# Kernel tuning notes

Hardware: AMD Instinct MI355X
Metric: run time of the kernel (lower is better)

## Reference

```python
import jax, jax.numpy as jnp
import numpy as np

N = 100000; E = 1600000; C = 32; H = 2
KS = (3, 3, 5, 5)
NEG = 0.01      # LeakyReLU default slope
GAT_NEG = 0.2   # SuperGAT attention leaky_relu slope
EPS = 1e-5      # BatchNorm eps


def setup_inputs() -> dict:
    key = jax.random.key(0)
    ks = jax.random.split(key, 64)
    inp = {}
    inp["patch_embs"] = jax.random.normal(ks[0], (N, C), dtype=jnp.float32)
    ei = np.array(jax.random.randint(ks[1], (2, E), 0, N))
    # avoid self loops so PyG's remove_self_loops/add_self_loops semantics match exactly
    ei[1] = np.where(ei[0] == ei[1], (ei[1] + 1) % N, ei[1])
    inp["edge_index"] = jnp.array(ei, dtype=jnp.int32)
    inp["edge_attr"] = jax.random.normal(ks[2], (E, 1), dtype=jnp.float32)
    s = 1.0 / np.sqrt(C)
    i = 3
    for b in range(4):
        inp[f"W{b}"] = (jax.random.normal(ks[i], (KS[b], C, C)) * s).astype(jnp.float32); i += 1
        inp[f"cb{b}"] = jnp.zeros((C,), jnp.float32)                     # ChebConv bias
        inp[f"G{b}"] = (jax.random.normal(ks[i], (C, H * C)) * s).astype(jnp.float32); i += 1  # SuperGAT lin
        inp[f"al{b}"] = (jax.random.normal(ks[i], (H, C)) * s).astype(jnp.float32); i += 1     # att_l
        inp[f"ar{b}"] = (jax.random.normal(ks[i], (H, C)) * s).astype(jnp.float32); i += 1     # att_r
        inp[f"gb{b}"] = jnp.zeros((C,), jnp.float32)                     # SuperGAT bias
        inp[f"gm{b}"] = jnp.ones((C,), jnp.float32)                      # BN gamma
        inp[f"bt{b}"] = jnp.zeros((C,), jnp.float32)                     # BN beta
    return inp


def _cheb(x, src, dst, w, W, cb):
    # ChebConv with sym Laplacian, lambda_max=2 -> L_hat = -D^-1/2 A D^-1/2
    def spmv(v):
        return jax.ops.segment_sum(w[:, None] * v[src], dst, num_segments=N)
    tx0, out = x, x @ W[0]
    tx1 = spmv(x)
    out = out + tx1 @ W[1]
    for k in range(2, W.shape[0]):
        tx0, tx1 = tx1, 2.0 * spmv(tx1) - tx0
        out = out + tx1 @ W[k]
    return out + cb


def _supergat(x, ssrc, sdst, G, al, ar, gb):
    # SuperGATConv, attention_type='MX', heads=2, concat=False (mean)
    h = (x @ G).reshape(N, H, C)          # [N,H,C]
    hi, hj = h[sdst], h[ssrc]              # gathered per edge (incl. self loops)
    logits = jnp.sum(hi * hj, -1)          # [Etot,H]
    a = jnp.sum(hj * al, -1) + jnp.sum(hi * ar, -1)
    a = jax.nn.leaky_relu(a * jax.nn.sigmoid(logits), GAT_NEG)
    amax = jax.ops.segment_max(a, sdst, num_segments=N)
    ex = jnp.exp(a - amax[sdst])
    den = jax.ops.segment_sum(ex, sdst, num_segments=N)
    alpha = ex / (den[sdst] + 1e-16)
    out = jax.ops.segment_sum(alpha[..., None] * hj, sdst, num_segments=N)
    return out.mean(axis=1) + gb


def _block(x, src, dst, w, ssrc, sdst, W, cb, G, al, ar, gb, gm, bt):
    s_ = _supergat(_cheb(x, src, dst, w, W, cb), ssrc, sdst, G, al, ar, gb)
    y = jax.nn.leaky_relu(s_, NEG) + s_
    mu = y.mean(0)
    var = y.var(0)  # biased var, matches torch BN training normalization
    return gm * (y - mu) / jnp.sqrt(var + EPS) + bt


def _forward(x, edge_index, params):
    src, dst = edge_index[0], edge_index[1]
    deg = jax.ops.segment_sum(jnp.ones((E,), jnp.float32), src, num_segments=N)
    di = deg[src] * deg[dst]
    w = jnp.where(di > 0, -1.0 / jnp.sqrt(jnp.maximum(di, 1e-12)), 0.0)
    loop = jnp.arange(N, dtype=edge_index.dtype)
    ssrc = jnp.concatenate([src, loop])
    sdst = jnp.concatenate([dst, loop])
    acc = 0.0
    for b in range(4):
        W, cb, G, al, ar, gb, gm, bt = params[b]
        acc = acc + _block(x, src, dst, w, ssrc, sdst, W, cb, G, al, ar, gb, gm, bt)
    return jax.nn.leaky_relu(acc, NEG)


def reference(patch_embs, edge_index, edge_attr,
              W0, cb0, G0, al0, ar0, gb0, gm0, bt0,
              W1, cb1, G1, al1, ar1, gb1, gm1, bt1,
              W2, cb2, G2, al2, ar2, gb2, gm2, bt2,
              W3, cb3, G3, al3, ar3, gb3, gm3, bt3):
    params = [(W0, cb0, G0, al0, ar0, gb0, gm0, bt0),
              (W1, cb1, G1, al1, ar1, gb1, gm1, bt1),
              (W2, cb2, G2, al2, ar2, gb2, gm2, bt2),
              (W3, cb3, G3, al3, ar3, gb3, gm3, bt3)]
    return _forward(patch_embs, edge_index, params)
```

## Files before the change

kernel.cpp:

```cpp
#include <hip/hip_runtime.h>
#include <math.h>

#define NN 100000
#define EE 1600000
#define CCH 32
#define NC (NN*CCH)
#define ET (EE+NN)
#define NEGS 0.01f
#define GNEG 0.2f
#define BEPS 1e-5f


__global__ void k_degs(const int* __restrict__ src, const int* __restrict__ dst,
                       float* __restrict__ deg_out, int* __restrict__ indeg){
    int e = blockIdx.x*blockDim.x + threadIdx.x;
    if (e >= EE) return;
    atomicAdd(&deg_out[src[e]], 1.0f);
    atomicAdd(&indeg[dst[e]], 1);
}

#define SCAN_T 1024
__global__ void k_scan(const int* __restrict__ indeg, int* __restrict__ row){
    __shared__ int sdata[SCAN_T];
    int t = threadIdx.x;
    const int per = (NN + SCAN_T - 1)/SCAN_T;
    int lo = t*per, hi = (lo + per < NN) ? lo + per : NN;
    int s = 0;
    for (int d = lo; d < hi; d++) s += indeg[d] + 1;
    sdata[t] = s;
    __syncthreads();
    for (int off = 1; off < SCAN_T; off <<= 1){
        int v = (t >= off) ? sdata[t-off] : 0;
        __syncthreads();
        sdata[t] += v;
        __syncthreads();
    }
    int excl = (t == 0) ? 0 : sdata[t-1];
    for (int d = lo; d < hi; d++){
        row[d] = excl;
        excl += indeg[d] + 1;
    }
    if (t == 0) row[NN] = ET;
}

__global__ void k_self(const int* __restrict__ row, int* __restrict__ csr_src,
                       float* __restrict__ csr_w){
    int d = blockIdx.x*blockDim.x + threadIdx.x;
    if (d >= NN) return;
    int p = row[d];
    csr_src[p] = d;
    csr_w[p] = 0.0f;
}

__global__ void k_scatter(const int* __restrict__ src, const int* __restrict__ dst,
                          const float* __restrict__ deg_out, const int* __restrict__ row,
                          int* __restrict__ cur, int* __restrict__ csr_src,
                          float* __restrict__ csr_w){
    int e = blockIdx.x*blockDim.x + threadIdx.x;
    if (e >= EE) return;
    int s = src[e], d = dst[e];
    int pos = row[d] + 1 + atomicAdd(&cur[d], 1);
    csr_src[pos] = s;
    float di = deg_out[s] * deg_out[d];
    csr_w[pos] = (di > 0.0f) ? (-1.0f / sqrtf(fmaxf(di, 1e-12f))) : 0.0f;
}

__global__ void k_spmv_csr(const int* __restrict__ row, const int* __restrict__ csr_src,
                           const float* __restrict__ csr_w, const float* __restrict__ v,
                           const float* __restrict__ tprev, float* __restrict__ out, int first){
    int gid = blockIdx.x*blockDim.x + threadIdx.x;
    int node = gid >> 6;
    if (node >= NN) return;
    int lane = gid & 63;
    int slot = lane >> 4;
    int l = lane & 15;
    const float2* V2 = (const float2*)v;
    int start = row[node] + 1, end = row[node+1];
    float2 acc = {0.0f, 0.0f};
    int p = start + slot;
    for (; p + 4 < end; p += 8){
        int s0 = csr_src[p], s1 = csr_src[p+4];
        float w0 = csr_w[p], w1 = csr_w[p+4];
        float2 v0 = V2[(size_t)s0*16 + l];
        float2 v1 = V2[(size_t)s1*16 + l];
        acc.x += w0*v0.x + w1*v1.x;
        acc.y += w0*v0.y + w1*v1.y;
    }
    if (p < end){
        float w0 = csr_w[p];
        float2 v0 = V2[(size_t)csr_src[p]*16 + l];
        acc.x += w0*v0.x;
        acc.y += w0*v0.y;
    }
    acc.x += __shfl_xor(acc.x, 32); acc.y += __shfl_xor(acc.y, 32);
    acc.x += __shfl_xor(acc.x, 16); acc.y += __shfl_xor(acc.y, 16);
    if (slot == 0){
        float2 r;
        if (first){
            r = acc;
        } else {
            float2 t = ((const float2*)tprev)[(size_t)node*16 + l];
            r.x = 2.0f*acc.x - t.x;
            r.y = 2.0f*acc.y - t.y;
        }
        ((float2*)out)[(size_t)node*16 + l] = r;
    }
}

__global__ void k_wg(const float* __restrict__ W, const float* __restrict__ cb,
                     const float* __restrict__ G, float* __restrict__ Wg,
                     float* __restrict__ cbg, int K){
    int t = blockIdx.x*blockDim.x + threadIdx.x;
    if (t < K*2048){
        int k = t >> 11, r = t & 2047;
        int i = r >> 6, j = r & 63;
        float s = 0.0f;
        #pragma unroll 8
        for (int q = 0; q < 32; q++) s += W[k*1024 + i*32 + q] * G[q*64 + j];
        Wg[t] = s;
    } else if (t < K*2048 + 64){
        int j = t - K*2048;
        float s = 0.0f;
        #pragma unroll 8
        for (int q = 0; q < 32; q++) s += cb[q] * G[q*64 + j];
        cbg[j] = s;
    }
}

__global__ void k_hfused(const float* __restrict__ T0, const float* __restrict__ T1,
                         const float* __restrict__ T2, const float* __restrict__ T3,
                         const float* __restrict__ T4,
                         const float* __restrict__ Wg, const float* __restrict__ cbg,
                         const float* __restrict__ al, const float* __restrict__ ar,
                         int K, int b, float* __restrict__ H4,
                         float* __restrict__ attL4, float* __restrict__ attR4){
    __shared__ float sW[5*2048];
    for (int i = threadIdx.x; i < K*2048; i += blockDim.x) sW[i] = Wg[i];
    __syncthreads();
    int gid = blockIdx.x*blockDim.x + threadIdx.x;
    int node = gid >> 6;
    if (node >= NN) return;
    int lane = gid & 63;
    int h = lane >> 5, c = lane & 31;
    const float* Ts[5] = {T0, T1, T2, T3, T4};
    float acc = cbg[lane];
    for (int k = 0; k < K; k++){
        float tv = Ts[k][(size_t)node*CCH + c];
        const float* wrow = &sW[k*2048];
        #pragma unroll
        for (int i = 0; i < 32; i++){
            float t = __shfl(tv, i);
            acc += t * wrow[i*64 + lane];
        }
    }
    H4[(size_t)node*256 + lane*4 + b] = acc;
    float va = acc * al[lane];
    float vr = acc * ar[lane];
    #pragma unroll
    for (int m = 16; m >= 1; m >>= 1){
        va += __shfl_xor(va, m);
        vr += __shfl_xor(vr, m);
    }
    if (c == 0){
        attL4[(size_t)node*8 + h*4 + b] = va;
        attR4[(size_t)node*8 + h*4 + b] = vr;
    }
}

__global__ __launch_bounds__(512)
void k_gat4(const int* __restrict__ row, const int* __restrict__ csr_src,
            const float* __restrict__ H4,
            const float* __restrict__ attL4, const float* __restrict__ attR4,
            const float* __restrict__ gb0, const float* __restrict__ gb1,
            const float* __restrict__ gb2, const float* __restrict__ gb3,
            float* __restrict__ y4, float* __restrict__ sums){
    int gid = blockIdx.x*blockDim.x + threadIdx.x;
    int node = gid >> 6;
    int lane = gid & 63;
    int wv_ = threadIdx.x >> 6;
    int h = lane >> 5, c = lane & 31;
    __shared__ float4 ssum[8*32], ssq[8*32];
    float4 yv = {0.0f, 0.0f, 0.0f, 0.0f};
    if (node < NN){
        float hiA[4], aiA[4], mA[4], denA[4], accA[4];
        {
            float4 t = *(const float4*)&H4[(size_t)node*256 + lane*4];
            hiA[0]=t.x; hiA[1]=t.y; hiA[2]=t.z; hiA[3]=t.w;
            float4 u = *(const float4*)&attR4[(size_t)node*8 + h*4];
            aiA[0]=u.x; aiA[1]=u.y; aiA[2]=u.z; aiA[3]=u.w;
        }
        #pragma unroll
        for (int k = 0; k < 4; k++){ mA[k] = -1e30f; denA[k] = 0.0f; accA[k] = 0.0f; }
        int start = row[node], end = row[node+1];
        int p = start;
        for (; p + 3 < end; p += 4){
            int s[4]; float hj[4][4], aL[4][4], lg[4][4];
            #pragma unroll
            for (int i = 0; i < 4; i++) s[i] = csr_src[p+i];
            #pragma unroll
            for (int i = 0; i < 4; i++){
                float4 t = *(const float4*)&H4[(size_t)s[i]*256 + lane*4];
                hj[i][0]=t.x; hj[i][1]=t.y; hj[i][2]=t.z; hj[i][3]=t.w;
                float4 u = *(const float4*)&attL4[(size_t)s[i]*8 + h*4];
                aL[i][0]=u.x; aL[i][1]=u.y; aL[i][2]=u.z; aL[i][3]=u.w;
            }
            #pragma unroll
            for (int i = 0; i < 4; i++)
                #pragma unroll
                for (int k = 0; k < 4; k++) lg[i][k] = hiA[k]*hj[i][k];
            #pragma unroll
            for (int mm = 16; mm >= 1; mm >>= 1)
                #pragma unroll
                for (int i = 0; i < 4; i++)
                    #pragma unroll
                    for (int k = 0; k < 4; k++) lg[i][k] += __shfl_xor(lg[i][k], mm);
            #pragma unroll
            for (int k = 0; k < 4; k++){
                float a0 = (aL[0][k] + aiA[k]) / (1.0f + __expf(-lg[0][k]));
                float a1 = (aL[1][k] + aiA[k]) / (1.0f + __expf(-lg[1][k]));
                float a2 = (aL[2][k] + aiA[k]) / (1.0f + __expf(-lg[2][k]));
                float a3 = (aL[3][k] + aiA[k]) / (1.0f + __expf(-lg[3][k]));
                a0 = (a0 > 0.0f) ? a0 : GNEG*a0;
                a1 = (a1 > 0.0f) ? a1 : GNEG*a1;
                a2 = (a2 > 0.0f) ? a2 : GNEG*a2;
                a3 = (a3 > 0.0f) ? a3 : GNEG*a3;
                float mn = fmaxf(fmaxf(mA[k], fmaxf(a0, a1)), fmaxf(a2, a3));
                float sc = __expf(mA[k] - mn);
                float w0 = __expf(a0 - mn), w1 = __expf(a1 - mn);
                float w2 = __expf(a2 - mn), w3 = __expf(a3 - mn);
                denA[k] = denA[k]*sc + ((w0 + w1) + (w2 + w3));
                accA[k] = accA[k]*sc + (w0*hj[0][k] + w1*hj[1][k]) + (w2*hj[2][k] + w3*hj[3][k]);
                mA[k] = mn;
            }
        }
        for (; p < end; p++){
            int s0 = csr_src[p];
            float hj0[4], aL0[4], lg0[4];
            float4 t = *(const float4*)&H4[(size_t)s0*256 + lane*4];
            hj0[0]=t.x; hj0[1]=t.y; hj0[2]=t.z; hj0[3]=t.w;
            float4 u = *(const float4*)&attL4[(size_t)s0*8 + h*4];
            aL0[0]=u.x; aL0[1]=u.y; aL0[2]=u.z; aL0[3]=u.w;
            #pragma unroll
            for (int k = 0; k < 4; k++) lg0[k] = hiA[k]*hj0[k];
            #pragma unroll
            for (int mm = 16; mm >= 1; mm >>= 1)
                #pragma unroll
                for (int k = 0; k < 4; k++) lg0[k] += __shfl_xor(lg0[k], mm);
            #pragma unroll
            for (int k = 0; k < 4; k++){
                float a0 = (aL0[k] + aiA[k]) / (1.0f + __expf(-lg0[k]));
                a0 = (a0 > 0.0f) ? a0 : GNEG*a0;
                float mn = fmaxf(mA[k], a0);
                float sc = __expf(mA[k] - mn);
                float w0 = __expf(a0 - mn);
                denA[k] = denA[k]*sc + w0;
                accA[k] = accA[k]*sc + w0*hj0[k];
                mA[k] = mn;
            }
        }
        float g[4];
        g[0] = gb0[c]; g[1] = gb1[c]; g[2] = gb2[c]; g[3] = gb3[c];
        float yo[4];
        #pragma unroll
        for (int k = 0; k < 4; k++){
            float accn = accA[k] / (denA[k] + 1e-16f);
            float s_ = 0.5f*(accn + __shfl_xor(accn, 32)) + g[k];
            yo[k] = (s_ > 0.0f) ? 2.0f*s_ : (1.0f + NEGS)*s_;
        }
        yv.x = yo[0]; yv.y = yo[1]; yv.z = yo[2]; yv.w = yo[3];
        if (h == 0) *(float4*)&y4[(size_t)node*128 + c*4] = yv;
    }
    if (h == 0){
        ssum[wv_*32 + c] = yv;
        float4 q = {yv.x*yv.x, yv.y*yv.y, yv.z*yv.z, yv.w*yv.w};
        ssq[wv_*32 + c] = q;
    }
    __syncthreads();
    if (threadIdx.x < 32){
        float4 s = {0,0,0,0}, q = {0,0,0,0};
        #pragma unroll
        for (int r = 0; r < 8; r++){
            float4 a = ssum[r*32 + threadIdx.x];
            float4 b = ssq[r*32 + threadIdx.x];
            s.x += a.x; s.y += a.y; s.z += a.z; s.w += a.w;
            q.x += b.x; q.y += b.y; q.z += b.z; q.w += b.w;
        }
        atomicAdd(&sums[  0 + threadIdx.x], s.x);
        atomicAdd(&sums[ 32 + threadIdx.x], s.y);
        atomicAdd(&sums[ 64 + threadIdx.x], s.z);
        atomicAdd(&sums[ 96 + threadIdx.x], s.w);
        atomicAdd(&sums[128 + threadIdx.x], q.x);
        atomicAdd(&sums[160 + threadIdx.x], q.y);
        atomicAdd(&sums[192 + threadIdx.x], q.z);
        atomicAdd(&sums[224 + threadIdx.x], q.w);
    }
}

__global__ void k_norm4(const float* __restrict__ y4, const float* __restrict__ sums,
                        const float* __restrict__ gm0, const float* __restrict__ bt0,
                        const float* __restrict__ gm1, const float* __restrict__ bt1,
                        const float* __restrict__ gm2, const float* __restrict__ bt2,
                        const float* __restrict__ gm3, const float* __restrict__ bt3,
                        float* __restrict__ out){
    int t = blockIdx.x*blockDim.x + threadIdx.x;
    if (t >= NC) return;
    int c = t & 31;
    const float invN = 1.0f / (float)NN;
    float4 v = *(const float4*)&y4[(size_t)t*4];
    float r = 0.0f;
    {
        float mu = sums[c]*invN;       float var = sums[128+c]*invN - mu*mu;
        r += gm0[c]*(v.x - mu)/sqrtf(var + BEPS) + bt0[c];
    }
    {
        float mu = sums[32+c]*invN;    float var = sums[160+c]*invN - mu*mu;
        r += gm1[c]*(v.y - mu)/sqrtf(var + BEPS) + bt1[c];
    }
    {
        float mu = sums[64+c]*invN;    float var = sums[192+c]*invN - mu*mu;
        r += gm2[c]*(v.z - mu)/sqrtf(var + BEPS) + bt2[c];
    }
    {
        float mu = sums[96+c]*invN;    float var = sums[224+c]*invN - mu*mu;
        r += gm3[c]*(v.w - mu)/sqrtf(var + BEPS) + bt3[c];
    }
    out[t] = (r > 0.0f) ? r : NEGS*r;
}

extern "C" void kernel_launch(void* const* d_in, const int* in_sizes, int n_in,
                              void* d_out, int out_size, void* d_ws, size_t ws_size,
                              hipStream_t stream){
    const float* x   = (const float*)d_in[0];
    const int*   ei  = (const int*)d_in[1];
    const int*   src = ei;
    const int*   dst = ei + EE;

    const float *Wp[4], *cbp[4], *Gp[4], *alp[4], *arp[4], *gbp[4], *gmp[4], *btp[4];
    for (int b = 0; b < 4; b++){
        int base = 3 + 8*b;
        Wp[b]  = (const float*)d_in[base+0];
        cbp[b] = (const float*)d_in[base+1];
        Gp[b]  = (const float*)d_in[base+2];
        alp[b] = (const float*)d_in[base+3];
        arp[b] = (const float*)d_in[base+4];
        gbp[b] = (const float*)d_in[base+5];
        gmp[b] = (const float*)d_in[base+6];
        btp[b] = (const float*)d_in[base+7];
    }

    char* w8 = (char*)d_ws;
    #define CARVE(ptr_t, name, bytes) ptr_t name = (ptr_t)w8; w8 += (((size_t)(bytes)) + 15) & ~(size_t)15;
    CARVE(float*, deg_out, sizeof(float)*NN)
    CARVE(int*,   indeg,   sizeof(int)*NN)
    CARVE(int*,   cur,     sizeof(int)*NN)
    CARVE(int*,   row,     sizeof(int)*(NN+1))
    CARVE(int*,   csr_src, sizeof(int)*ET)
    CARVE(float*, csr_w,   sizeof(float)*ET)
    CARVE(float*, T1,      sizeof(float)*NC)
    CARVE(float*, T2,      sizeof(float)*NC)
    CARVE(float*, T3,      sizeof(float)*NC)
    CARVE(float*, T4,      sizeof(float)*NC)
    CARVE(float*, H4,      sizeof(float)*(size_t)NN*256)
    CARVE(float*, attL4,   sizeof(float)*NN*8)
    CARVE(float*, attR4,   sizeof(float)*NN*8)
    CARVE(float*, Wg,      sizeof(float)*4*5*2048)
    CARVE(float*, cbg,     sizeof(float)*4*64)
    CARVE(float*, sums,    sizeof(float)*256)
    float* y4 = T1;

    float* acc = (float*)d_out;

    const int B = 256;
    const int gE  = (EE + B - 1)/B;
    const int gN  = (NN + B - 1)/B;
    const int gNC = (NC + B - 1)/B;
    const int gW5 = (NN*64 + 511)/512;

    hipMemsetAsync(deg_out, 0, (size_t)3*NN*sizeof(int), stream);
    k_degs<<<gE, B, 0, stream>>>(src, dst, deg_out, indeg);
    k_scan<<<1, SCAN_T, 0, stream>>>(indeg, row);
    k_self<<<gN, B, 0, stream>>>(row, csr_src, csr_w);
    k_scatter<<<gE, B, 0, stream>>>(src, dst, deg_out, row, cur, csr_src, csr_w);

    k_spmv_csr<<<gW5, 512, 0, stream>>>(row, csr_src, csr_w, x,  (const float*)0, T1, 1);
    k_spmv_csr<<<gW5, 512, 0, stream>>>(row, csr_src, csr_w, T1, x,  T2, 0);
    k_spmv_csr<<<gW5, 512, 0, stream>>>(row, csr_src, csr_w, T2, T1, T3, 0);
    k_spmv_csr<<<gW5, 512, 0, stream>>>(row, csr_src, csr_w, T3, T2, T4, 0);

    const int Ks[4] = {3, 3, 5, 5};
    for (int b = 0; b < 4; b++){
        int tot = Ks[b]*2048 + 64;
        k_wg<<<(tot + B - 1)/B, B, 0, stream>>>(Wp[b], cbp[b], Gp[b],
                                                Wg + b*5*2048, cbg + b*64, Ks[b]);
    }

    for (int b = 0; b < 4; b++){
        k_hfused<<<gW5, 512, 0, stream>>>(x, T1, T2, T3, T4, Wg + b*5*2048, cbg + b*64,
                                          alp[b], arp[b], Ks[b], b, H4, attL4, attR4);
    }

    hipMemsetAsync(sums, 0, 256*sizeof(float), stream);
    k_gat4<<<gW5, 512, 0, stream>>>(row, csr_src, H4, attL4, attR4,
                                    gbp[0], gbp[1], gbp[2], gbp[3], y4, sums);

    k_norm4<<<gNC, B, 0, stream>>>(y4, sums,
                                   gmp[0], btp[0], gmp[1], btp[1],
                                   gmp[2], btp[2], gmp[3], btp[3], acc);
}
```

Before: 2.334 ms.

## Pre-scale CSR indices to byte offsets, use ds_swizzle reductions and fast rcp

Result: faster. 2.105 ms (-9.8%).

```diff
diff --git a/kernel.cpp b/kernel.cpp
--- a/kernel.cpp
+++ b/kernel.cpp
@@ -9,6 +9,10 @@
 #define NEGS 0.01f
 #define GNEG 0.2f
 #define BEPS 1e-5f
+
+#define DSWZ(x, pat) __int_as_float(__builtin_amdgcn_ds_swizzle(__float_as_int(x), pat))
+#define RED32(v) do{ v += DSWZ(v,0x041F); v += DSWZ(v,0x081F); v += DSWZ(v,0x101F); \
+                     v += DSWZ(v,0x201F); v += DSWZ(v,0x401F); }while(0)
 
 
 __global__ void k_degs(const int* __restrict__ src, const int* __restrict__ dst,
@@ -43,29 +47,29 @@
     if (t == 0) row[NN] = ET;
 }
 
-__global__ void k_self(const int* __restrict__ row, int* __restrict__ csr_src,
+__global__ void k_self(const int* __restrict__ row, int* __restrict__ csr_srcb,
                        float* __restrict__ csr_w){
     int d = blockIdx.x*blockDim.x + threadIdx.x;
     if (d >= NN) return;
     int p = row[d];
-    csr_src[p] = d;
+    csr_srcb[p] = d << 7;
     csr_w[p] = 0.0f;
 }
 
 __global__ void k_scatter(const int* __restrict__ src, const int* __restrict__ dst,
                           const float* __restrict__ deg_out, const int* __restrict__ row,
-                          int* __restrict__ cur, int* __restrict__ csr_src,
+                          int* __restrict__ cur, int* __restrict__ csr_srcb,
                           float* __restrict__ csr_w){
     int e = blockIdx.x*blockDim.x + threadIdx.x;
     if (e >= EE) return;
     int s = src[e], d = dst[e];
     int pos = row[d] + 1 + atomicAdd(&cur[d], 1);
-    csr_src[pos] = s;
+    csr_srcb[pos] = s << 7;
     float di = deg_out[s] * deg_out[d];
-    csr_w[pos] = (di > 0.0f) ? (-1.0f / sqrtf(fmaxf(di, 1e-12f))) : 0.0f;
-}
-
-__global__ void k_spmv_csr(const int* __restrict__ row, const int* __restrict__ csr_src,
+    csr_w[pos] = (di > 0.0f) ? (-__frsqrt_rn(fmaxf(di, 1e-12f))) : 0.0f;
+}
+
+__global__ void k_spmv_csr(const int* __restrict__ row, const int* __restrict__ csr_srcb,
                            const float* __restrict__ csr_w, const float* __restrict__ v,
                            const float* __restrict__ tprev, float* __restrict__ out, int first){
     int gid = blockIdx.x*blockDim.x + threadIdx.x;
@@ -74,26 +78,28 @@
     int lane = gid & 63;
     int slot = lane >> 4;
     int l = lane & 15;
-    const float2* V2 = (const float2*)v;
+    const char* vb = (const char*)v + (l << 3);
     int start = row[node] + 1, end = row[node+1];
     float2 acc = {0.0f, 0.0f};
     int p = start + slot;
-    for (; p + 4 < end; p += 8){
-        int s0 = csr_src[p], s1 = csr_src[p+4];
-        float w0 = csr_w[p], w1 = csr_w[p+4];
-        float2 v0 = V2[(size_t)s0*16 + l];
-        float2 v1 = V2[(size_t)s1*16 + l];
-        acc.x += w0*v0.x + w1*v1.x;
-        acc.y += w0*v0.y + w1*v1.y;
-    }
-    if (p < end){
+    for (; p + 12 < end; p += 16){
+        int b0 = csr_srcb[p], b1 = csr_srcb[p+4], b2 = csr_srcb[p+8], b3 = csr_srcb[p+12];
+        float w0 = csr_w[p], w1 = csr_w[p+4], w2 = csr_w[p+8], w3 = csr_w[p+12];
+        float2 v0 = *(const float2*)(vb + (size_t)(unsigned)b0);
+        float2 v1 = *(const float2*)(vb + (size_t)(unsigned)b1);
+        float2 v2 = *(const float2*)(vb + (size_t)(unsigned)b2);
+        float2 v3 = *(const float2*)(vb + (size_t)(unsigned)b3);
+        acc.x += w0*v0.x + w1*v1.x + w2*v2.x + w3*v3.x;
+        acc.y += w0*v0.y + w1*v1.y + w2*v2.y + w3*v3.y;
+    }
+    for (; p < end; p += 4){
         float w0 = csr_w[p];
-        float2 v0 = V2[(size_t)csr_src[p]*16 + l];
+        float2 v0 = *(const float2*)(vb + (size_t)(unsigned)csr_srcb[p]);
         acc.x += w0*v0.x;
         acc.y += w0*v0.y;
     }
     acc.x += __shfl_xor(acc.x, 32); acc.y += __shfl_xor(acc.y, 32);
-    acc.x += __shfl_xor(acc.x, 16); acc.y += __shfl_xor(acc.y, 16);
+    acc.x += DSWZ(acc.x, 0x401F);  acc.y += DSWZ(acc.y, 0x401F);
     if (slot == 0){
         float2 r;
         if (first){
@@ -156,11 +162,8 @@
     H4[(size_t)node*256 + lane*4 + b] = acc;
     float va = acc * al[lane];
     float vr = acc * ar[lane];
-    #pragma unroll
-    for (int m = 16; m >= 1; m >>= 1){
-        va += __shfl_xor(va, m);
-        vr += __shfl_xor(vr, m);
-    }
+    RED32(va);
+    RED32(vr);
     if (c == 0){
         attL4[(size_t)node*8 + h*4 + b] = va;
         attR4[(size_t)node*8 + h*4 + b] = vr;
@@ -168,7 +171,7 @@
 }
 
 __global__ __launch_bounds__(512)
-void k_gat4(const int* __restrict__ row, const int* __restrict__ csr_src,
+void k_gat4(const int* __restrict__ row, const int* __restrict__ csr_srcb,
             const float* __restrict__ H4,
             const float* __restrict__ attL4, const float* __restrict__ attR4,
             const float* __restrict__ gb0, const float* __restrict__ gb1,
@@ -179,6 +182,8 @@
     int lane = gid & 63;
     int wv_ = threadIdx.x >> 6;
     int h = lane >> 5, c = lane & 31;
+    const char* Hb = (const char*)H4 + (lane << 4);
+    const char* Lb = (const char*)attL4 + (h << 4);
     __shared__ float4 ssum[8*32], ssq[8*32];
     float4 yv = {0.0f, 0.0f, 0.0f, 0.0f};
     if (node < NN){
@@ -194,14 +199,14 @@
         int start = row[node], end = row[node+1];
         int p = start;
         for (; p + 3 < end; p += 4){
-            int s[4]; float hj[4][4], aL[4][4], lg[4][4];
-            #pragma unroll
-            for (int i = 0; i < 4; i++) s[i] = csr_src[p+i];
+            int sb[4]; float hj[4][4], aL[4][4], lg[4][4];
+            #pragma unroll
+            for (int i = 0; i < 4; i++) sb[i] = csr_srcb[p+i];
             #pragma unroll
             for (int i = 0; i < 4; i++){
-                float4 t = *(const float4*)&H4[(size_t)s[i]*256 + lane*4];
+                float4 t = *(const float4*)(Hb + ((size_t)(unsigned)sb[i] << 3));
                 hj[i][0]=t.x; hj[i][1]=t.y; hj[i][2]=t.z; hj[i][3]=t.w;
-                float4 u = *(const float4*)&attL4[(size_t)s[i]*8 + h*4];
+                float4 u = *(const float4*)(Lb + (size_t)(unsigned)(sb[i] >> 2));
                 aL[i][0]=u.x; aL[i][1]=u.y; aL[i][2]=u.z; aL[i][3]=u.w;
             }
             #pragma unroll
@@ -209,21 +214,19 @@
                 #pragma unroll
                 for (int k = 0; k < 4; k++) lg[i][k] = hiA[k]*hj[i][k];
             #pragma unroll
-            for (int mm = 16; mm >= 1; mm >>= 1)
+            for (int i = 0; i < 4; i++)
                 #pragma unroll
-                for (int i = 0; i < 4; i++)
-                    #pragma unroll
-                    for (int k = 0; k < 4; k++) lg[i][k] += __shfl_xor(lg[i][k], mm);
+                for (int k = 0; k < 4; k++) RED32(lg[i][k]);
             #pragma unroll
             for (int k = 0; k < 4; k++){
-                float a0 = (aL[0][k] + aiA[k]) / (1.0f + __expf(-lg[0][k]));
-                float a1 = (aL[1][k] + aiA[k]) / (1.0f + __expf(-lg[1][k]));
-                float a2 = (aL[2][k] + aiA[k]) / (1.0f + __expf(-lg[2][k]));
-                float a3 = (aL[3][k] + aiA[k]) / (1.0f + __expf(-lg[3][k]));
-                a0 = (a0 > 0.0f) ? a0 : GNEG*a0;
-                a1 = (a1 > 0.0f) ? a1 : GNEG*a1;
-                a2 = (a2 > 0.0f) ? a2 : GNEG*a2;
-                a3 = (a3 > 0.0f) ? a3 : GNEG*a3;
+                float a0 = (aL[0][k] + aiA[k]) * __builtin_amdgcn_rcpf(1.0f + __expf(-lg[0][k]));
+                float a1 = (aL[1][k] + aiA[k]) * __builtin_amdgcn_rcpf(1.0f + __expf(-lg[1][k]));
+                float a2 = (aL[2][k] + aiA[k]) * __builtin_amdgcn_rcpf(1.0f + __expf(-lg[2][k]));
+                float a3 = (aL[3][k] + aiA[k]) * __builtin_amdgcn_rcpf(1.0f + __expf(-lg[3][k]));
+                a0 = fmaxf(a0, GNEG*a0);
+                a1 = fmaxf(a1, GNEG*a1);
+                a2 = fmaxf(a2, GNEG*a2);
+                a3 = fmaxf(a3, GNEG*a3);
                 float mn = fmaxf(fmaxf(mA[k], fmaxf(a0, a1)), fmaxf(a2, a3));
                 float sc = __expf(mA[k] - mn);
                 float w0 = __expf(a0 - mn), w1 = __expf(a1 - mn);
@@ -234,22 +237,20 @@
             }
         }
         for (; p < end; p++){
-            int s0 = csr_src[p];
+            int sb0 = csr_srcb[p];
             float hj0[4], aL0[4], lg0[4];
-            float4 t = *(const float4*)&H4[(size_t)s0*256 + lane*4];
+            float4 t = *(const float4*)(Hb + ((size_t)(unsigned)sb0 << 3));
             hj0[0]=t.x; hj0[1]=t.y; hj0[2]=t.z; hj0[3]=t.w;
-            float4 u = *(const float4*)&attL4[(size_t)s0*8 + h*4];
+            float4 u = *(const float4*)(Lb + (size_t)(unsigned)(sb0 >> 2));
             aL0[0]=u.x; aL0[1]=u.y; aL0[2]=u.z; aL0[3]=u.w;
             #pragma unroll
             for (int k = 0; k < 4; k++) lg0[k] = hiA[k]*hj0[k];
             #pragma unroll
-            for (int mm = 16; mm >= 1; mm >>= 1)
-                #pragma unroll
-                for (int k = 0; k < 4; k++) lg0[k] += __shfl_xor(lg0[k], mm);
+            for (int k = 0; k < 4; k++) RED32(lg0[k]);
             #pragma unroll
             for (int k = 0; k < 4; k++){
-                float a0 = (aL0[k] + aiA[k]) / (1.0f + __expf(-lg0[k]));
-                a0 = (a0 > 0.0f) ? a0 : GNEG*a0;
+                float a0 = (aL0[k] + aiA[k]) * __builtin_amdgcn_rcpf(1.0f + __expf(-lg0[k]));
+                a0 = fmaxf(a0, GNEG*a0);
                 float mn = fmaxf(mA[k], a0);
                 float sc = __expf(mA[k] - mn);
                 float w0 = __expf(a0 - mn);
@@ -263,7 +264,7 @@
         float yo[4];
         #pragma unroll
         for (int k = 0; k < 4; k++){
-            float accn = accA[k] / (denA[k] + 1e-16f);
+            float accn = accA[k] * __builtin_amdgcn_rcpf(denA[k] + 1e-16f);
             float s_ = 0.5f*(accn + __shfl_xor(accn, 32)) + g[k];
             yo[k] = (s_ > 0.0f) ? 2.0f*s_ : (1.0f + NEGS)*s_;
         }
@@ -354,7 +355,7 @@
     CARVE(int*,   indeg,   sizeof(int)*NN)
     CARVE(int*,   cur,     sizeof(int)*NN)
     CARVE(int*,   row,     sizeof(int)*(NN+1))
-    CARVE(int*,   csr_src, sizeof(int)*ET)
+    CARVE(int*,   csr_srcb, sizeof(int)*ET)
     CARVE(float*, csr_w,   sizeof(float)*ET)
     CARVE(float*, T1,      sizeof(float)*NC)
     CARVE(float*, T2,      sizeof(float)*NC)
@@ -379,13 +380,13 @@
     hipMemsetAsync(deg_out, 0, (size_t)3*NN*sizeof(int), stream);
     k_degs<<<gE, B, 0, stream>>>(src, dst, deg_out, indeg);
     k_scan<<<1, SCAN_T, 0, stream>>>(indeg, row);
-    k_self<<<gN, B, 0, stream>>>(row, csr_src, csr_w);
-    k_scatter<<<gE, B, 0, stream>>>(src, dst, deg_out, row, cur, csr_src, csr_w);
-
-    k_spmv_csr<<<gW5, 512, 0, stream>>>(row, csr_src, csr_w, x,  (const float*)0, T1, 1);
-    k_spmv_csr<<<gW5, 512, 0, stream>>>(row, csr_src, csr_w, T1, x,  T2, 0);
-    k_spmv_csr<<<gW5, 512, 0, stream>>>(row, csr_src, csr_w, T2, T1, T3, 0);
-    k_spmv_csr<<<gW5, 512, 0, stream>>>(row, csr_src, csr_w, T3, T2, T4, 0);
+    k_self<<<gN, B, 0, stream>>>(row, csr_srcb, csr_w);
+    k_scatter<<<gE, B, 0, stream>>>(src, dst, deg_out, row, cur, csr_srcb, csr_w);
+
+    k_spmv_csr<<<gW5, 512, 0, stream>>>(row, csr_srcb, csr_w, x,  (const float*)0, T1, 1);
+    k_spmv_csr<<<gW5, 512, 0, stream>>>(row, csr_srcb, csr_w, T1, x,  T2, 0);
+    k_spmv_csr<<<gW5, 512, 0, stream>>>(row, csr_srcb, csr_w, T2, T1, T3, 0);
+    k_spmv_csr<<<gW5, 512, 0, stream>>>(row, csr_srcb, csr_w, T3, T2, T4, 0);
 
     const int Ks[4] = {3, 3, 5, 5};
     for (int b = 0; b < 4; b++){
@@ -400,7 +401,7 @@
     }
 
     hipMemsetAsync(sums, 0, 256*sizeof(float), stream);
-    k_gat4<<<gW5, 512, 0, stream>>>(row, csr_src, H4, attL4, attR4,
+    k_gat4<<<gW5, 512, 0, stream>>>(row, csr_srcb, H4, attL4, attR4,
                                     gbp[0], gbp[1], gbp[2], gbp[3], y4, sums);
 
     k_norm4<<<gNC, B, 0, stream>>>(y4, sums,
```
